# Kernel tuning notes

Measured on AMD Instinct MI355X. Metric: run time of the kernel, lower is better.

## Reference

```python
import jax, jax.numpy as jnp
import numpy as np

DIM = 512
NUM_HEADS = 8
HEAD_DIM = DIM // NUM_HEADS
SCALE = HEAD_DIM ** -0.5


def setup_inputs() -> dict:
    key = jax.random.key(0)
    ks = jax.random.split(key, 5)
    B, D, H, W, C = 2, 8, 16, 16, DIM
    x = jax.random.normal(ks[0], (B, D, H, W, C), dtype=jnp.float32)
    # torch Linear params stored as [in, out] so y = x @ W + b
    qkv_w = jax.random.normal(ks[1], (C, 3 * C), dtype=jnp.float32) * (C ** -0.5)
    qkv_b = jax.random.normal(ks[2], (3 * C,), dtype=jnp.float32) * 0.02
    proj_w = jax.random.normal(ks[3], (C, C), dtype=jnp.float32) * (C ** -0.5)
    proj_b = jax.random.normal(ks[4], (C,), dtype=jnp.float32) * 0.02
    return {"x": x, "qkv_w": qkv_w, "qkv_b": qkv_b, "proj_w": proj_w, "proj_b": proj_b}


def reference(x, qkv_w, qkv_b, proj_w, proj_b):
    B, D, H, W, C = x.shape
    N = D * H * W
    x_flat = x.reshape(B, N, C)
    qkv = (x_flat @ qkv_w + qkv_b).reshape(B, N, 3, NUM_HEADS, HEAD_DIM)
    qkv = jnp.transpose(qkv, (2, 0, 3, 1, 4))  # [3, B, h, N, hd]
    q, k, v = qkv[0], qkv[1], qkv[2]
    attn = jnp.einsum('bhnd,bhmd->bhnm', q, k) * SCALE  # [B, h, N, N]
    attn = jnp.clip(attn, -10000.0, 10000.0)
    attn = jax.nn.softmax(attn, axis=-1)
    attn = jnp.nan_to_num(attn, nan=0.0)
    out = jnp.einsum('bhnm,bhmd->bhnd', attn, v)  # [B, h, N, hd]
    out = jnp.transpose(out, (0, 2, 1, 3)).reshape(B, N, C)
    out = out @ proj_w + proj_b
    return out.reshape(B, D, H, W, C)
```

## Files before the change

kernel.cpp:

```cpp
#include <hip/hip_runtime.h>
#include <stdint.h>

typedef unsigned short u16;
typedef __bf16 bf16x8 __attribute__((ext_vector_type(8)));
typedef _Float16 f16x4 __attribute__((ext_vector_type(4)));
typedef _Float16 f16x8 __attribute__((ext_vector_type(8)));
typedef float  f32x4  __attribute__((ext_vector_type(4)));

__device__ __forceinline__ u16 f2bf(float f) {
  union { float f; unsigned u; } v; v.f = f;
  unsigned r = v.u + 0x7FFFu + ((v.u >> 16) & 1u);
  return (u16)(r >> 16);
}

__device__ __forceinline__ void gload16(const void* g, void* l) {
  __builtin_amdgcn_global_load_lds((const __attribute__((address_space(1))) unsigned int*)g,
                                   (__attribute__((address_space(3))) unsigned int*)l, 16, 0, 0);
}

__device__ __forceinline__ f32x4 mfma32(bf16x8 a, bf16x8 b, f32x4 c) {
  return __builtin_amdgcn_mfma_f32_16x16x32_bf16(a, b, c, 0, 0, 0);
}

__global__ void k_prep(const float* __restrict__ x, const float* __restrict__ qw,
                       const float* __restrict__ pjw, u16* __restrict__ Xb,
                       u16* __restrict__ Wt, u16* __restrict__ Pt) {
  __shared__ u16 tile[64][65];
  const int b = blockIdx.x, t = threadIdx.x;
  if (b < 2048) {
    int i = b * 256 + t;
    float4 v = ((const float4*)x)[i];
    uint2 o;
    o.x = (unsigned)f2bf(v.x) | ((unsigned)f2bf(v.y) << 16);
    o.y = (unsigned)f2bf(v.z) | ((unsigned)f2bf(v.w) << 16);
    ((uint2*)Xb)[i] = o;
    return;
  }
  const float* in; u16* out; int Cc, bx, by;
  if (b < 2240) { in = qw;  out = Wt; Cc = 1536; bx = (b - 2048) % 24; by = (b - 2048) / 24; }
  else          { in = pjw; out = Pt; Cc = 512;  bx = (b - 2240) & 7;  by = (b - 2240) >> 3; }
  const int c0 = bx * 64, r0 = by * 64;
  #pragma unroll
  for (int i = 0; i < 16; ++i) {
    int idx = t + i * 256;
    int r = idx >> 6, c = idx & 63;
    tile[c][r] = f2bf(in[(size_t)(r0 + r) * Cc + c0 + c]);
  }
  __syncthreads();
  #pragma unroll
  for (int i = 0; i < 16; ++i) {
    int idx = t + i * 256;
    int r = idx >> 6, c = idx & 63;
    out[(size_t)(c0 + r) * 512 + r0 + c] = tile[r][c];
  }
}

__device__ __forceinline__ int swz64(int row, int colByte) {
  return (row * 128 + (colByte ^ ((row & 7) << 4))) >> 1;
}
__device__ __forceinline__ int swzK(int row, int colByte) {
  return (row * 128 + (colByte ^ ((row & 3) << 4) ^ (((row >> 3) & 1) << 6))) >> 1;
}

template<int BM, int BN>
__device__ __forceinline__ void gemm_core(const u16* __restrict__ A, const u16* __restrict__ Bt,
                                          int m0, int n0, f32x4 (&acc)[BM/32][BN/32],
                                          u16* lA, u16* lB) {
  const int t = threadIdx.x;
  const int lane = t & 63;
  const int w = t >> 6, wr = w >> 1, wc = w & 1;
  const int lr = lane & 15, lg = lane >> 4;
  const int r0 = t >> 3, j0 = t & 7;
  const int cA = (j0 ^ (r0 & 7)) * 8;
  #pragma unroll 1
  for (int k0 = 0; k0 < 512; k0 += 64) {
    __syncthreads();
    #pragma unroll
    for (int u = 0; u < BM / 32; ++u)
      gload16(A + (size_t)(m0 + u * 32 + r0) * 512 + k0 + cA, (char*)lA + u * 4096 + w * 1024);
    #pragma unroll
    for (int u = 0; u < BN / 32; ++u)
      gload16(Bt + (size_t)(n0 + u * 32 + r0) * 512 + k0 + cA, (char*)lB + u * 4096 + w * 1024);
    __syncthreads();
    #pragma unroll
    for (int kh = 0; kh < 2; ++kh) {
      bf16x8 af[BM / 32], bfr[BN / 32];
      #pragma unroll
      for (int i = 0; i < BM / 32; ++i)
        af[i] = __builtin_bit_cast(bf16x8, *(const uint4*)&lA[swz64(wr * (BM / 2) + i * 16 + lr, kh * 64 + lg * 16)]);
      #pragma unroll
      for (int j = 0; j < BN / 32; ++j)
        bfr[j] = __builtin_bit_cast(bf16x8, *(const uint4*)&lB[swz64(wc * (BN / 2) + j * 16 + lr, kh * 64 + lg * 16)]);
      #pragma unroll
      for (int i = 0; i < BM / 32; ++i)
        #pragma unroll
        for (int j = 0; j < BN / 32; ++j)
          acc[i][j] = mfma32(af[i], bfr[j], acc[i][j]);
    }
  }
}

__global__ __launch_bounds__(256, 2) void k_gemm_qkv(const u16* __restrict__ A, const u16* __restrict__ Bt,
                                                     const float* __restrict__ bias,
                                                     u16* __restrict__ Qb, u16* __restrict__ Kb,
                                                     u16* __restrict__ Vtb) {
  __shared__ __align__(16) u16 lA[128 * 64];
  __shared__ __align__(16) u16 lB[64 * 64];
  __shared__ __align__(16) u16 vt[9216];
  f32x4 acc[4][2];
  #pragma unroll
  for (int i = 0; i < 4; ++i)
    #pragma unroll
    for (int j = 0; j < 2; ++j) acc[i][j] = (f32x4){0.f, 0.f, 0.f, 0.f};
  const int m0 = blockIdx.x * 128, n0 = blockIdx.y * 64;
  gemm_core<128, 64>(A, Bt, m0, n0, acc, lA, lB);
  const int t = threadIdx.x;
  const int lane = t & 63;
  const int w = t >> 6, wr = w >> 1, wc = w & 1;
  const int lr = lane & 15, lg = lane >> 4;
  const int which = n0 >> 9, h = (n0 >> 6) & 7;
  const int b = m0 >> 11, m0l = m0 & 2047;
  const size_t bh = (size_t)(b * 8 + h);
  if (which != 2) {
    const float scl = (which == 0) ? 0.18033688011112042f : 1.0f;
    #pragma unroll
    for (int i = 0; i < 4; ++i)
      #pragma unroll
      for (int j = 0; j < 2; ++j) {
        int n = n0 + wc * 32 + j * 16 + lr;
        float bb = bias[n];
        #pragma unroll
        for (int r = 0; r < 4; ++r)
          vt[(wr * 64 + i * 16 + lg * 4 + r) * 72 + wc * 32 + j * 16 + lr] =
              f2bf((acc[i][j][r] + bb) * scl);
      }
    __syncthreads();
    u16* dst = (which == 0 ? Qb : Kb) + (bh * 2048 + m0l) * 64;
    #pragma unroll
    for (int it = 0; it < 4; ++it) {
      int unit = it * 256 + t, row = unit >> 3, ch = unit & 7;
      *(uint4*)&dst[row * 64 + ch * 8] = *(const uint4*)&vt[row * 72 + ch * 8];
    }
  } else {
    #pragma unroll
    for (int i = 0; i < 4; ++i)
      #pragma unroll
      for (int j = 0; j < 2; ++j) {
        int n = n0 + wc * 32 + j * 16 + lr;
        float bb = bias[n];
        uint2 pk;
        pk.x = (unsigned)f2bf(acc[i][j][0] + bb) | ((unsigned)f2bf(acc[i][j][1] + bb) << 16);
        pk.y = (unsigned)f2bf(acc[i][j][2] + bb) | ((unsigned)f2bf(acc[i][j][3] + bb) << 16);
        *(uint2*)&vt[(wc * 32 + j * 16 + lr) * 136 + wr * 64 + i * 16 + lg * 4] = pk;
      }
    __syncthreads();
    u16* dst = Vtb + bh * 64 * 2048 + m0l;
    #pragma unroll
    for (int it = 0; it < 4; ++it) {
      int unit = it * 256 + t, row = unit >> 4, ch = unit & 15;
      *(uint4*)&dst[(size_t)row * 2048 + ch * 8] = *(const uint4*)&vt[row * 136 + ch * 8];
    }
  }
}

__global__ __launch_bounds__(256, 2) void k_gemm_proj(const u16* __restrict__ A, const u16* __restrict__ Bt,
                                                      const float* __restrict__ bias,
                                                      float* __restrict__ out) {
  __shared__ __align__(16) u16 lA[64 * 64];
  __shared__ __align__(16) u16 lB[64 * 64];
  f32x4 acc[2][2];
  #pragma unroll
  for (int i = 0; i < 2; ++i)
    #pragma unroll
    for (int j = 0; j < 2; ++j) acc[i][j] = (f32x4){0.f, 0.f, 0.f, 0.f};
  const int m0 = blockIdx.x * 64, n0 = blockIdx.y * 64;
  gemm_core<64, 64>(A, Bt, m0, n0, acc, lA, lB);
  const int lane = threadIdx.x & 63;
  const int w = threadIdx.x >> 6, wr = w >> 1, wc = w & 1;
  const int lr = lane & 15, lg = lane >> 4;
  #pragma unroll
  for (int i = 0; i < 2; ++i)
    #pragma unroll
    for (int j = 0; j < 2; ++j)
      #pragma unroll
      for (int r = 0; r < 4; ++r) {
        int m = m0 + wr * 32 + i * 16 + lg * 4 + r;
        int n = n0 + wc * 32 + j * 16 + lr;
        out[(size_t)m * 512 + n] = acc[i][j][r] + bias[n];
      }
}

__global__ __launch_bounds__(512, 4) void k_attn(const u16* __restrict__ Qb, const u16* __restrict__ Kb,
                                                 const u16* __restrict__ Vtb,
                                                 u16* __restrict__ Op, float* __restrict__ Lp) {
  __shared__ __align__(16) u16 smem[32768];
  const int t = threadIdx.x;
  const int lane = t & 63, w = t >> 6;
  const int lr = lane & 15, lg = lane >> 4;
  const int f = blockIdx.x;
  const int xc = f & 7, jj = f >> 3;
  const int group = xc + ((jj >> 3) << 3);
  const int qtile = jj & 7, bh = group & 15, split = group >> 4;
  const int q0 = qtile * 256 + w * 32;
  const int sBeg = split * 512;

  bf16x8 qf[2][2];
  #pragma unroll
  for (int c = 0; c < 2; ++c) {
    const u16* qrow = Qb + ((size_t)bh * 2048 + q0 + c * 16 + lr) * 64;
    qf[c][0] = __builtin_bit_cast(bf16x8, *(const uint4*)(qrow + lg * 8));
    qf[c][1] = __builtin_bit_cast(bf16x8, *(const uint4*)(qrow + 32 + lg * 8));
  }

  f32x4 oacc[2][4], lacc[2];
  #pragma unroll
  for (int c = 0; c < 2; ++c) {
    lacc[c] = (f32x4){0.f, 0.f, 0.f, 0.f};
    #pragma unroll
    for (int ff = 0; ff < 4; ++ff) oacc[c][ff] = (f32x4){0.f, 0.f, 0.f, 0.f};
  }
  bf16x8 ones8;
  #pragma unroll
  for (int k = 0; k < 8; ++k) ones8[k] = (__bf16)1.f;
  const f32x4 NEG12 = (f32x4){-12.f, -12.f, -12.f, -12.f};

  const int prowBase = ((lr >> 2) << 3) + (lr & 3);

  const int r0 = t >> 3, j0 = t & 7;
  const int cK = (j0 ^ ((r0 & 3) | (((r0 >> 3) & 1) << 2))) * 8;
  const int cV = (j0 ^ (r0 & 7)) * 8;
  const u16* Kbase = Kb + (size_t)bh * 2048 * 64;
  const u16* Vbase = Vtb + (size_t)bh * 64 * 2048;
  const u16* kg = Kbase + (size_t)(sBeg + r0) * 64 + cK;
  const u16* vg = Vbase + (size_t)r0 * 2048 + sBeg + cV;

  auto STAGE = [&](int slot) {
    gload16(kg, smem + slot * 4096 + w * 512);
    gload16(vg, smem + 16384 + slot * 4096 + w * 512);
    kg += 4096; vg += 64;
  };

  auto COMPUTE = [&](int slot) {
    const u16* KC = smem + slot * 4096;
    const u16* VC = smem + 16384 + slot * 4096;
    #pragma unroll
    for (int j32 = 0; j32 < 2; ++j32) {
      f32x4 sa[2][2];
      __builtin_amdgcn_s_setprio(1);
      #pragma unroll
      for (int p = 0; p < 2; ++p) {
        const int prow = j32 * 32 + p * 4 + prowBase;
        bf16x8 kb0 = __builtin_bit_cast(bf16x8, *(const uint4*)&KC[swzK(prow, lg * 16)]);
        bf16x8 kb1 = __builtin_bit_cast(bf16x8, *(const uint4*)&KC[swzK(prow, 64 + lg * 16)]);
        #pragma unroll
        for (int c = 0; c < 2; ++c) {
          f32x4 z = mfma32(kb0, qf[c][0], NEG12);
          sa[c][p] = mfma32(kb1, qf[c][1], z);
        }
      }
      __builtin_amdgcn_s_setprio(0);
      bf16x8 pb[2];
      #pragma unroll
      for (int c = 0; c < 2; ++c)
        #pragma unroll
        for (int p = 0; p < 2; ++p)
          #pragma unroll
          for (int r = 0; r < 4; ++r)
            pb[c][p * 4 + r] = (__bf16)exp2f(sa[c][p][r]);
      __builtin_amdgcn_s_setprio(1);
      lacc[0] = mfma32(ones8, pb[0], lacc[0]);
      lacc[1] = mfma32(ones8, pb[1], lacc[1]);
      #pragma unroll
      for (int ff = 0; ff < 4; ++ff) {
        bf16x8 va = __builtin_bit_cast(bf16x8, *(const uint4*)&VC[swz64(ff * 16 + lr, j32 * 64 + lg * 16)]);
        oacc[0][ff] = mfma32(va, pb[0], oacc[0][ff]);
        oacc[1][ff] = mfma32(va, pb[1], oacc[1][ff]);
      }
      __builtin_amdgcn_s_setprio(0);
    }
  };

  STAGE(0); STAGE(1);
  #pragma unroll 1
  for (int pp = 0; pp < 4; ++pp) {
    const int sA = (pp & 1) * 2;
    __syncthreads();
    if (pp < 3) { STAGE(sA ^ 2); STAGE((sA ^ 2) + 1); }
    COMPUTE(sA);
    COMPUTE(sA + 1);
  }

  __syncthreads();
  #pragma unroll
  for (int c = 0; c < 2; ++c) {
    const int ql = w * 32 + c * 16 + lr;
    #pragma unroll
    for (int ff = 0; ff < 4; ++ff) {
      f16x4 hv;
      hv[0] = (_Float16)oacc[c][ff][0]; hv[1] = (_Float16)oacc[c][ff][1];
      hv[2] = (_Float16)oacc[c][ff][2]; hv[3] = (_Float16)oacc[c][ff][3];
      *(uint2*)&smem[ql * 72 + ff * 16 + lg * 4] = __builtin_bit_cast(uint2, hv);
    }
  }
  __syncthreads();
  {
    u16* dst = Op + ((size_t)(split * 16 + bh) * 2048 + qtile * 256) * 64;
    #pragma unroll
    for (int it = 0; it < 4; ++it) {
      int unit = it * 512 + t, row = unit >> 3, ch = unit & 7;
      *(uint4*)&dst[row * 64 + ch * 8] = *(const uint4*)&smem[row * 72 + ch * 8];
    }
  }
  #pragma unroll
  for (int c = 0; c < 2; ++c) {
    if (lg == 0) {
      const size_t orow = (size_t)((split * 16 + bh) * 2048) + q0 + c * 16 + lr;
      Lp[orow] = lacc[c][0];
    }
  }
}

__global__ void k_combine(const u16* __restrict__ Op, const float* __restrict__ Lp,
                          u16* __restrict__ AO) {
  int idx = blockIdx.x * 256 + threadIdx.x;
  int chunk = idx & 7, row = idx >> 3;
  float den = Lp[row] + Lp[32768 + row] + Lp[65536 + row] + Lp[98304 + row];
  float inv = 1.0f / den;
  float o[8];
  #pragma unroll
  for (int k = 0; k < 8; ++k) o[k] = 0.f;
  #pragma unroll
  for (int s = 0; s < 4; ++s) {
    uint4 u = ((const uint4*)Op)[(size_t)s * 262144 + row * 8 + chunk];
    f16x8 hv = __builtin_bit_cast(f16x8, u);
    #pragma unroll
    for (int k = 0; k < 8; ++k) o[k] += (float)hv[k];
  }
  bf16x8 bv;
  #pragma unroll
  for (int k = 0; k < 8; ++k) bv[k] = (__bf16)(o[k] * inv);
  int bh = row >> 11, q = row & 2047, bb = bh >> 3, h = bh & 7;
  *(uint4*)&AO[((size_t)(bb * 2048 + q)) * 512 + h * 64 + chunk * 8] = __builtin_bit_cast(uint4, bv);
}

extern "C" void kernel_launch(void* const* d_in, const int* in_sizes, int n_in,
                              void* d_out, int out_size, void* d_ws, size_t ws_size,
                              hipStream_t stream) {
  (void)in_sizes; (void)n_in; (void)out_size; (void)ws_size;
  const float* x      = (const float*)d_in[0];
  const float* qkv_w  = (const float*)d_in[1];
  const float* qkv_b  = (const float*)d_in[2];
  const float* proj_w = (const float*)d_in[3];
  const float* proj_b = (const float*)d_in[4];
  float* out = (float*)d_out;
  char* wsc = (char*)d_ws;
  float* Lp  = (float*)(wsc + 0);
  u16*   Xb  = (u16*)(wsc + 0);
  u16*   Wt  = (u16*)(wsc + 4194304);
  u16*   Pt  = (u16*)(wsc + 5767168);
  u16*   Qb  = (u16*)(wsc + 6291456);
  u16*   Kb  = (u16*)(wsc + 10485760);
  u16*   Vtb = (u16*)(wsc + 14680064);
  u16*   AO  = (u16*)(wsc + 18874368);
  u16*   Op  = (u16*)(wsc + 23068672);

  k_prep<<<2304, 256, 0, stream>>>(x, qkv_w, proj_w, Xb, Wt, Pt);
  k_gemm_qkv<<<dim3(32, 24), 256, 0, stream>>>(Xb, Wt, qkv_b, Qb, Kb, Vtb);
  k_attn<<<512, 512, 0, stream>>>(Qb, Kb, Vtb, Op, Lp);
  k_combine<<<1024, 256, 0, stream>>>(Op, Lp, AO);
  k_gemm_proj<<<dim3(64, 8), 256, 0, stream>>>(AO, Pt, proj_b, out);
}
```

Baseline: 60.64 us.

## Double-buffer GEMM LDS stages and fuse split-KV combine into projection GEMM

The shared GEMM core now double-buffers its LDS tiles, issuing the next K-slice's global-to-LDS loads before computing on the current one, which removes one barrier per iteration. The separate combine kernel is removed: the projection GEMM reads the four fp16 split-KV partial outputs and their softmax denominators directly, normalises and converts them to bf16 in registers, and writes them into LDS as its A operand, prefetching the next slice during the current MFMAs. This saves a kernel launch and a round trip of the attention output through global memory. In exchange, each of the 8 column blocks of the projection re-reads and re-combines the same partials, LDS use doubles, and register pressure rises.

```diff
diff --git a/kernel.cpp b/kernel.cpp
--- a/kernel.cpp
+++ b/kernel.cpp
@@ -63,7 +63,7 @@
 }
 
 template<int BM, int BN>
-__device__ __forceinline__ void gemm_core(const u16* __restrict__ A, const u16* __restrict__ Bt,
+__device__ __forceinline__ void gemm_pipe(const u16* __restrict__ A, const u16* __restrict__ Bt,
                                           int m0, int n0, f32x4 (&acc)[BM/32][BN/32],
                                           u16* lA, u16* lB) {
   const int t = threadIdx.x;
@@ -72,25 +72,33 @@
   const int lr = lane & 15, lg = lane >> 4;
   const int r0 = t >> 3, j0 = t & 7;
   const int cA = (j0 ^ (r0 & 7)) * 8;
+  auto STAGE = [&](int buf, int k0) {
+    char* dA = (char*)lA + buf * (BM * 128);
+    char* dB = (char*)lB + buf * (BN * 128);
+    #pragma unroll
+    for (int u = 0; u < BM / 32; ++u)
+      gload16(A + (size_t)(m0 + u * 32 + r0) * 512 + k0 + cA, dA + u * 4096 + w * 1024);
+    #pragma unroll
+    for (int u = 0; u < BN / 32; ++u)
+      gload16(Bt + (size_t)(n0 + u * 32 + r0) * 512 + k0 + cA, dB + u * 4096 + w * 1024);
+  };
+  STAGE(0, 0);
   #pragma unroll 1
   for (int k0 = 0; k0 < 512; k0 += 64) {
+    const int buf = (k0 >> 6) & 1;
     __syncthreads();
-    #pragma unroll
-    for (int u = 0; u < BM / 32; ++u)
-      gload16(A + (size_t)(m0 + u * 32 + r0) * 512 + k0 + cA, (char*)lA + u * 4096 + w * 1024);
-    #pragma unroll
-    for (int u = 0; u < BN / 32; ++u)
-      gload16(Bt + (size_t)(n0 + u * 32 + r0) * 512 + k0 + cA, (char*)lB + u * 4096 + w * 1024);
-    __syncthreads();
+    if (k0 + 64 < 512) STAGE(buf ^ 1, k0 + 64);
+    const u16* sA = lA + buf * (BM * 64);
+    const u16* sB = lB + buf * (BN * 64);
     #pragma unroll
     for (int kh = 0; kh < 2; ++kh) {
       bf16x8 af[BM / 32], bfr[BN / 32];
       #pragma unroll
       for (int i = 0; i < BM / 32; ++i)
-        af[i] = __builtin_bit_cast(bf16x8, *(const uint4*)&lA[swz64(wr * (BM / 2) + i * 16 + lr, kh * 64 + lg * 16)]);
+        af[i] = __builtin_bit_cast(bf16x8, *(const uint4*)&sA[swz64(wr * (BM / 2) + i * 16 + lr, kh * 64 + lg * 16)]);
       #pragma unroll
       for (int j = 0; j < BN / 32; ++j)
-        bfr[j] = __builtin_bit_cast(bf16x8, *(const uint4*)&lB[swz64(wc * (BN / 2) + j * 16 + lr, kh * 64 + lg * 16)]);
+        bfr[j] = __builtin_bit_cast(bf16x8, *(const uint4*)&sB[swz64(wc * (BN / 2) + j * 16 + lr, kh * 64 + lg * 16)]);
       #pragma unroll
       for (int i = 0; i < BM / 32; ++i)
         #pragma unroll
@@ -104,8 +112,8 @@
                                                      const float* __restrict__ bias,
                                                      u16* __restrict__ Qb, u16* __restrict__ Kb,
                                                      u16* __restrict__ Vtb) {
-  __shared__ __align__(16) u16 lA[128 * 64];
-  __shared__ __align__(16) u16 lB[64 * 64];
+  __shared__ __align__(16) u16 lA[2 * 128 * 64];
+  __shared__ __align__(16) u16 lB[2 * 64 * 64];
   __shared__ __align__(16) u16 vt[9216];
   f32x4 acc[4][2];
   #pragma unroll
@@ -113,7 +121,7 @@
     #pragma unroll
     for (int j = 0; j < 2; ++j) acc[i][j] = (f32x4){0.f, 0.f, 0.f, 0.f};
   const int m0 = blockIdx.x * 128, n0 = blockIdx.y * 64;
-  gemm_core<128, 64>(A, Bt, m0, n0, acc, lA, lB);
+  gemm_pipe<128, 64>(A, Bt, m0, n0, acc, lA, lB);
   const int t = threadIdx.x;
   const int lane = t & 63;
   const int w = t >> 6, wr = w >> 1, wc = w & 1;
@@ -163,21 +171,91 @@
   }
 }
 
-__global__ __launch_bounds__(256, 2) void k_gemm_proj(const u16* __restrict__ A, const u16* __restrict__ Bt,
+__global__ __launch_bounds__(256, 2) void k_gemm_proj(const u16* __restrict__ Op,
+                                                      const float* __restrict__ Lp,
+                                                      const u16* __restrict__ Bt,
                                                       const float* __restrict__ bias,
                                                       float* __restrict__ out) {
-  __shared__ __align__(16) u16 lA[64 * 64];
-  __shared__ __align__(16) u16 lB[64 * 64];
+  __shared__ __align__(16) u16 lA[2 * 64 * 64];
+  __shared__ __align__(16) u16 lB[2 * 64 * 64];
   f32x4 acc[2][2];
   #pragma unroll
   for (int i = 0; i < 2; ++i)
     #pragma unroll
     for (int j = 0; j < 2; ++j) acc[i][j] = (f32x4){0.f, 0.f, 0.f, 0.f};
   const int m0 = blockIdx.x * 64, n0 = blockIdx.y * 64;
-  gemm_core<64, 64>(A, Bt, m0, n0, acc, lA, lB);
-  const int lane = threadIdx.x & 63;
-  const int w = threadIdx.x >> 6, wr = w >> 1, wc = w & 1;
+  const int t = threadIdx.x;
+  const int lane = t & 63;
+  const int w = t >> 6, wr = w >> 1, wc = w & 1;
   const int lr = lane & 15, lg = lane >> 4;
+  const int r0 = t >> 3, j0 = t & 7;
+  const int cB = (j0 ^ (r0 & 7)) * 8;
+  const int b = m0 >> 11, q0l = m0 & 2047;
+
+  uint4 av[2][4];
+  float lv[2][4];
+  auto LOAD_A = [&](int k0) {
+    const int bh = b * 8 + (k0 >> 6);
+    #pragma unroll
+    for (int i = 0; i < 2; ++i) {
+      int u = t + i * 256, row = u >> 3, ch = u & 7;
+      const size_t rbase = (size_t)bh * 2048 + q0l + row;
+      #pragma unroll
+      for (int s = 0; s < 4; ++s) {
+        av[i][s] = *(const uint4*)(Op + ((size_t)s * 32768 + rbase) * 64 + ch * 8);
+        lv[i][s] = Lp[(size_t)s * 32768 + rbase];
+      }
+    }
+  };
+  auto WRITE_A = [&](int buf) {
+    #pragma unroll
+    for (int i = 0; i < 2; ++i) {
+      int u = t + i * 256, row = u >> 3, ch = u & 7;
+      float inv = 1.0f / (lv[i][0] + lv[i][1] + lv[i][2] + lv[i][3]);
+      f16x8 h0 = __builtin_bit_cast(f16x8, av[i][0]);
+      f16x8 h1 = __builtin_bit_cast(f16x8, av[i][1]);
+      f16x8 h2 = __builtin_bit_cast(f16x8, av[i][2]);
+      f16x8 h3 = __builtin_bit_cast(f16x8, av[i][3]);
+      bf16x8 bv;
+      #pragma unroll
+      for (int k = 0; k < 8; ++k)
+        bv[k] = (__bf16)(((float)h0[k] + (float)h1[k] + (float)h2[k] + (float)h3[k]) * inv);
+      *(uint4*)&lA[buf * 4096 + swz64(row, ch * 16)] = __builtin_bit_cast(uint4, bv);
+    }
+  };
+  auto STAGE_B = [&](int buf, int k0) {
+    char* dB = (char*)lB + buf * 8192;
+    gload16(Bt + (size_t)(n0 + r0) * 512 + k0 + cB, dB + w * 1024);
+    gload16(Bt + (size_t)(n0 + 32 + r0) * 512 + k0 + cB, dB + 4096 + w * 1024);
+  };
+
+  LOAD_A(0);
+  STAGE_B(0, 0);
+  WRITE_A(0);
+  #pragma unroll 1
+  for (int k0 = 0; k0 < 512; k0 += 64) {
+    const int buf = (k0 >> 6) & 1;
+    __syncthreads();
+    if (k0 + 64 < 512) { STAGE_B(buf ^ 1, k0 + 64); LOAD_A(k0 + 64); }
+    const u16* sA = lA + buf * 4096;
+    const u16* sB = lB + buf * 4096;
+    #pragma unroll
+    for (int kh = 0; kh < 2; ++kh) {
+      bf16x8 af[2], bfr[2];
+      #pragma unroll
+      for (int i = 0; i < 2; ++i)
+        af[i] = __builtin_bit_cast(bf16x8, *(const uint4*)&sA[swz64(wr * 32 + i * 16 + lr, kh * 64 + lg * 16)]);
+      #pragma unroll
+      for (int j = 0; j < 2; ++j)
+        bfr[j] = __builtin_bit_cast(bf16x8, *(const uint4*)&sB[swz64(wc * 32 + j * 16 + lr, kh * 64 + lg * 16)]);
+      #pragma unroll
+      for (int i = 0; i < 2; ++i)
+        #pragma unroll
+        for (int j = 0; j < 2; ++j)
+          acc[i][j] = mfma32(af[i], bfr[j], acc[i][j]);
+    }
+    if (k0 + 64 < 512) WRITE_A(buf ^ 1);
+  }
   #pragma unroll
   for (int i = 0; i < 2; ++i)
     #pragma unroll
@@ -318,29 +396,6 @@
       Lp[orow] = lacc[c][0];
     }
   }
-}
-
-__global__ void k_combine(const u16* __restrict__ Op, const float* __restrict__ Lp,
-                          u16* __restrict__ AO) {
-  int idx = blockIdx.x * 256 + threadIdx.x;
-  int chunk = idx & 7, row = idx >> 3;
-  float den = Lp[row] + Lp[32768 + row] + Lp[65536 + row] + Lp[98304 + row];
-  float inv = 1.0f / den;
-  float o[8];
-  #pragma unroll
-  for (int k = 0; k < 8; ++k) o[k] = 0.f;
-  #pragma unroll
-  for (int s = 0; s < 4; ++s) {
-    uint4 u = ((const uint4*)Op)[(size_t)s * 262144 + row * 8 + chunk];
-    f16x8 hv = __builtin_bit_cast(f16x8, u);
-    #pragma unroll
-    for (int k = 0; k < 8; ++k) o[k] += (float)hv[k];
-  }
-  bf16x8 bv;
-  #pragma unroll
-  for (int k = 0; k < 8; ++k) bv[k] = (__bf16)(o[k] * inv);
-  int bh = row >> 11, q = row & 2047, bb = bh >> 3, h = bh & 7;
-  *(uint4*)&AO[((size_t)(bb * 2048 + q)) * 512 + h * 64 + chunk * 8] = __builtin_bit_cast(uint4, bv);
 }
 
 extern "C" void kernel_launch(void* const* d_in, const int* in_sizes, int n_in,
@@ -361,12 +416,10 @@
   u16*   Qb  = (u16*)(wsc + 6291456);
   u16*   Kb  = (u16*)(wsc + 10485760);
   u16*   Vtb = (u16*)(wsc + 14680064);
-  u16*   AO  = (u16*)(wsc + 18874368);
   u16*   Op  = (u16*)(wsc + 23068672);
 
   k_prep<<<2304, 256, 0, stream>>>(x, qkv_w, proj_w, Xb, Wt, Pt);
   k_gemm_qkv<<<dim3(32, 24), 256, 0, stream>>>(Xb, Wt, qkv_b, Qb, Kb, Vtb);
   k_attn<<<512, 512, 0, stream>>>(Qb, Kb, Vtb, Op, Lp);
-  k_combine<<<1024, 256, 0, stream>>>(Op, Lp, AO);
-  k_gemm_proj<<<dim3(64, 8), 256, 0, stream>>>(AO, Pt, proj_b, out);
-}
+  k_gemm_proj<<<dim3(64, 8), 256, 0, stream>>>(Op, Lp, Pt, proj_b, out);
+}
```

Result: slower. 65.70 us (+8.4%).

## Double-buffer LDS tiles in QKV and projection GEMM main loops

Applied to the files above, without the earlier changes.

Replaces the single-buffered GEMM K-loop with a two-stage ping-pong. The next 64-wide K tile is loaded asynchronously into the alternate LDS buffer while MFMAs consume the current one, and one barrier per iteration is removed. The goal is to hide global-to-LDS load latency behind compute in both linear-layer kernels. The cost is double the LDS per block, which could reduce occupancy in the QKV kernel that also holds a transpose buffer.

```diff
diff --git a/kernel.cpp b/kernel.cpp
--- a/kernel.cpp
+++ b/kernel.cpp
@@ -63,7 +63,7 @@
 }
 
 template<int BM, int BN>
-__device__ __forceinline__ void gemm_core(const u16* __restrict__ A, const u16* __restrict__ Bt,
+__device__ __forceinline__ void gemm_pipe(const u16* __restrict__ A, const u16* __restrict__ Bt,
                                           int m0, int n0, f32x4 (&acc)[BM/32][BN/32],
                                           u16* lA, u16* lB) {
   const int t = threadIdx.x;
@@ -72,25 +72,33 @@
   const int lr = lane & 15, lg = lane >> 4;
   const int r0 = t >> 3, j0 = t & 7;
   const int cA = (j0 ^ (r0 & 7)) * 8;
+  auto STAGE = [&](int buf, int k0) {
+    char* dA = (char*)lA + buf * (BM * 128);
+    char* dB = (char*)lB + buf * (BN * 128);
+    #pragma unroll
+    for (int u = 0; u < BM / 32; ++u)
+      gload16(A + (size_t)(m0 + u * 32 + r0) * 512 + k0 + cA, dA + u * 4096 + w * 1024);
+    #pragma unroll
+    for (int u = 0; u < BN / 32; ++u)
+      gload16(Bt + (size_t)(n0 + u * 32 + r0) * 512 + k0 + cA, dB + u * 4096 + w * 1024);
+  };
+  STAGE(0, 0);
   #pragma unroll 1
   for (int k0 = 0; k0 < 512; k0 += 64) {
+    const int buf = (k0 >> 6) & 1;
     __syncthreads();
-    #pragma unroll
-    for (int u = 0; u < BM / 32; ++u)
-      gload16(A + (size_t)(m0 + u * 32 + r0) * 512 + k0 + cA, (char*)lA + u * 4096 + w * 1024);
-    #pragma unroll
-    for (int u = 0; u < BN / 32; ++u)
-      gload16(Bt + (size_t)(n0 + u * 32 + r0) * 512 + k0 + cA, (char*)lB + u * 4096 + w * 1024);
-    __syncthreads();
+    if (k0 + 64 < 512) STAGE(buf ^ 1, k0 + 64);
+    const u16* sA = lA + buf * (BM * 64);
+    const u16* sB = lB + buf * (BN * 64);
     #pragma unroll
     for (int kh = 0; kh < 2; ++kh) {
       bf16x8 af[BM / 32], bfr[BN / 32];
       #pragma unroll
       for (int i = 0; i < BM / 32; ++i)
-        af[i] = __builtin_bit_cast(bf16x8, *(const uint4*)&lA[swz64(wr * (BM / 2) + i * 16 + lr, kh * 64 + lg * 16)]);
+        af[i] = __builtin_bit_cast(bf16x8, *(const uint4*)&sA[swz64(wr * (BM / 2) + i * 16 + lr, kh * 64 + lg * 16)]);
       #pragma unroll
       for (int j = 0; j < BN / 32; ++j)
-        bfr[j] = __builtin_bit_cast(bf16x8, *(const uint4*)&lB[swz64(wc * (BN / 2) + j * 16 + lr, kh * 64 + lg * 16)]);
+        bfr[j] = __builtin_bit_cast(bf16x8, *(const uint4*)&sB[swz64(wc * (BN / 2) + j * 16 + lr, kh * 64 + lg * 16)]);
       #pragma unroll
       for (int i = 0; i < BM / 32; ++i)
         #pragma unroll
@@ -104,8 +112,8 @@
                                                      const float* __restrict__ bias,
                                                      u16* __restrict__ Qb, u16* __restrict__ Kb,
                                                      u16* __restrict__ Vtb) {
-  __shared__ __align__(16) u16 lA[128 * 64];
-  __shared__ __align__(16) u16 lB[64 * 64];
+  __shared__ __align__(16) u16 lA[2 * 128 * 64];
+  __shared__ __align__(16) u16 lB[2 * 64 * 64];
   __shared__ __align__(16) u16 vt[9216];
   f32x4 acc[4][2];
   #pragma unroll
@@ -113,7 +121,7 @@
     #pragma unroll
     for (int j = 0; j < 2; ++j) acc[i][j] = (f32x4){0.f, 0.f, 0.f, 0.f};
   const int m0 = blockIdx.x * 128, n0 = blockIdx.y * 64;
-  gemm_core<128, 64>(A, Bt, m0, n0, acc, lA, lB);
+  gemm_pipe<128, 64>(A, Bt, m0, n0, acc, lA, lB);
   const int t = threadIdx.x;
   const int lane = t & 63;
   const int w = t >> 6, wr = w >> 1, wc = w & 1;
@@ -166,15 +174,15 @@
 __global__ __launch_bounds__(256, 2) void k_gemm_proj(const u16* __restrict__ A, const u16* __restrict__ Bt,
                                                       const float* __restrict__ bias,
                                                       float* __restrict__ out) {
-  __shared__ __align__(16) u16 lA[64 * 64];
-  __shared__ __align__(16) u16 lB[64 * 64];
+  __shared__ __align__(16) u16 lA[2 * 64 * 64];
+  __shared__ __align__(16) u16 lB[2 * 64 * 64];
   f32x4 acc[2][2];
   #pragma unroll
   for (int i = 0; i < 2; ++i)
     #pragma unroll
     for (int j = 0; j < 2; ++j) acc[i][j] = (f32x4){0.f, 0.f, 0.f, 0.f};
   const int m0 = blockIdx.x * 64, n0 = blockIdx.y * 64;
-  gemm_core<64, 64>(A, Bt, m0, n0, acc, lA, lB);
+  gemm_pipe<64, 64>(A, Bt, m0, n0, acc, lA, lB);
   const int lane = threadIdx.x & 63;
   const int w = threadIdx.x >> 6, wr = w >> 1, wc = w & 1;
   const int lr = lane & 15, lg = lane >> 4;
```

Result: slower. 65.63 us (+8.2%).
